# Optimization experiments

Measured on AMD Instinct MI355X. Metric: run time of the kernel, lower is better.

## Reference

```python
import jax, jax.numpy as jnp
import numpy as np

N, L = 1, 384
NODE, H, PD = 256, 8, 128
HD = NODE // H
D1 = H * PD + NODE  # out_transform input dim = 1280


def instance_norm(x, eps=1e-5):
    # x: (N, C, H, W); torch InstanceNorm2d default: no affine, biased var
    m = x.mean(axis=(2, 3), keepdims=True)
    v = x.var(axis=(2, 3), keepdims=True)
    return (x - m) / jnp.sqrt(v + eps)


def conv3x3(x, w, b):
    y = jax.lax.conv_general_dilated(x, w, (1, 1), 'SAME',
                                     dimension_numbers=('NCHW', 'OIHW', 'NCHW'))
    return y + b[None, :, None, None]


def leaky(x):
    return jnp.where(x >= 0, x, 0.01 * x)


def layer_norm(x, w, b, eps=1e-5):
    m = x.mean(-1, keepdims=True)
    v = x.var(-1, keepdims=True)
    return (x - m) / jnp.sqrt(v + eps) * w + b


def setup_inputs() -> dict:
    key = jax.random.key(0)
    ks = jax.random.split(key, 32)
    s = 0.05
    inp = {
        'x': jax.random.normal(ks[0], (N, L, NODE), jnp.float32),
        'z': jax.random.normal(ks[1], (N, L, L, PD), jnp.float32),
        'plddt': jax.random.uniform(ks[2], (N, L, L, 1), jnp.float32),
        # linear weights stored (in, out) so application is x @ W
        'Wq': jax.random.normal(ks[3], (NODE, NODE), jnp.float32) * s,
        'Wk': jax.random.normal(ks[4], (NODE, NODE), jnp.float32) * s,
        'Wv': jax.random.normal(ks[5], (NODE, NODE), jnp.float32) * s,
        'Wp2a': jax.random.normal(ks[6], (PD, H), jnp.float32) * s,
        'conv_a_w': jax.random.normal(ks[7], (H, 2 * H, 3, 3), jnp.float32) * s,
        'conv_a_b': jnp.zeros((H,), jnp.float32),
        'conv_m_w': jax.random.normal(ks[8], (H, H + 1, 3, 3), jnp.float32) * s,
        'conv_m_b': jnp.zeros((H,), jnp.float32),
        'ln1_w': jnp.ones((D1,), jnp.float32),
        'ln1_b': jnp.zeros((D1,), jnp.float32),
        'lin1_w': jax.random.normal(ks[9], (D1, 2 * NODE), jnp.float32) * s,
        'lin1_b': jnp.zeros((2 * NODE,), jnp.float32),
        'ln2_w': jnp.ones((2 * NODE,), jnp.float32),
        'ln2_b': jnp.zeros((2 * NODE,), jnp.float32),
        'lin2_w': jax.random.normal(ks[10], (2 * NODE, NODE), jnp.float32) * s,
        'lin2_b': jnp.zeros((NODE,), jnp.float32),
        'lnf_w': jnp.ones((NODE,), jnp.float32),
        'lnf_b': jnp.zeros((NODE,), jnp.float32),
        'conv_p_w': jax.random.normal(ks[11], (PD, H + PD, 3, 3), jnp.float32) * s,
        'conv_p_b': jnp.zeros((PD,), jnp.float32),
    }
    return inp


def reference(x, z, plddt, Wq, Wk, Wv, Wp2a, conv_a_w, conv_a_b, conv_m_w,
              conv_m_b, ln1_w, ln1_b, lin1_w, lin1_b, ln2_w, ln2_b, lin2_w,
              lin2_b, lnf_w, lnf_b, conv_p_w, conv_p_b):
    Nb, Lh, D = x.shape
    nh = conv_a_w.shape[0]
    hd = D // nh
    Pd = z.shape[-1]
    # node -> alpha (GAT-style QK scores per head)
    q = (x @ Wq).reshape(Nb, Lh, nh, hd)
    k = (x @ Wk).reshape(Nb, Lh, nh, hd)
    v = (x @ Wv).reshape(Nb, Lh, nh, hd)
    a_node = jnp.einsum('nlhd,nmhd->nlmh', q, k) / jnp.sqrt(jnp.float32(hd))
    a_pair = z @ Wp2a                                  # (N,L,L,H)
    a = jnp.concatenate([a_pair, a_node], -1).transpose(0, 3, 1, 2)  # (N,2H,L,L)
    a = leaky(conv3x3(instance_norm(a), conv_a_w, conv_a_b))
    a = jnp.concatenate([a, plddt.transpose(0, 3, 1, 2)], 1)          # (N,H+1,L,L)
    a = leaky(conv3x3(instance_norm(a), conv_m_w, conv_m_b))
    a = a.transpose(0, 2, 3, 1)                                        # (N,L,L,H)
    # aggregations
    nfn = jnp.einsum('nlmh,nmhd->nlhd', a, v).reshape(Nb, Lh, D)       # node from node
    nfp = jnp.einsum('nlmh,nlmp->nlhp', a, z).reshape(Nb, Lh, nh * Pd) # node from pair
    cat = jnp.concatenate([nfp, nfn], -1)
    h = layer_norm(cat, ln1_w, ln1_b) @ lin1_w + lin1_b
    h = leaky(layer_norm(h, ln2_w, ln2_b)) @ lin2_w + lin2_b
    x_new = layer_norm(x + h, lnf_w, lnf_b)
    zp = jnp.concatenate([z, a], -1).transpose(0, 3, 1, 2)             # (N,P+H,L,L)
    z_new = leaky(conv3x3(instance_norm(zp), conv_p_w, conv_p_b)).transpose(0, 2, 3, 1)
    return x_new, z_new
```

## Files before the change

kernel.cpp:

```cpp
#include <hip/hip_runtime.h>
#include <stdint.h>

#define LSEQ 384
#define LL   147456
#define NODE 256
#define NH   8
#define HD   32
#define PDIM 128
#define D1   1280
#define D2   512

typedef __attribute__((ext_vector_type(8))) short s16x8;
typedef __attribute__((ext_vector_type(8))) __bf16 bf16x8;
typedef __attribute__((ext_vector_type(4))) float f32x4;

__device__ __forceinline__ float bf2f(uint16_t u) {
    union { uint32_t i; float f; } x; x.i = ((uint32_t)u) << 16; return x.f;
}
__device__ __forceinline__ uint16_t f2bf(float f) {
    uint32_t b = __float_as_uint(f);
    return (uint16_t)((b + 0x7FFFu + ((b >> 16) & 1u)) >> 16);
}
__device__ __forceinline__ float ld(const void* p, size_t i, int bf) {
    return bf ? bf2f(((const uint16_t*)p)[i]) : ((const float*)p)[i];
}
__device__ __forceinline__ void stout(void* p, size_t i, float v, int bf) {
    if (bf) ((uint16_t*)p)[i] = f2bf(v);
    else    ((float*)p)[i] = v;
}

__device__ __forceinline__ bf16x8 bf16x8_zero() {
    union { s16x8 s; bf16x8 b; } u; u.s = (s16x8)0; return u.b;
}

__device__ __forceinline__ void block_reduce2_256(float* s1, float* s2, int t) {
    __syncthreads();
    for (int o = 128; o > 0; o >>= 1) {
        if (t < o) { s1[t] += s1[t + o]; s2[t] += s2[t + o]; }
        __syncthreads();
    }
}

__device__ __forceinline__ void acc8(uint4 u, float& s, float& ss) {
    uint32_t w[4] = { u.x, u.y, u.z, u.w };
    #pragma unroll
    for (int i = 0; i < 4; ++i) {
        float a = bf2f((uint16_t)(w[i] & 0xFFFFu));
        float b = bf2f((uint16_t)(w[i] >> 16));
        s += a + b;
        ss = fmaf(a, a, ss);
        ss = fmaf(b, b, ss);
    }
}

__global__ void k_detect(const uint32_t* __restrict__ zz, int* __restrict__ flag) {
    if (threadIdx.x == 0 && blockIdx.x == 0) {
        int cnt = 0;
        for (int i = 0; i < 256; ++i) {
            uint32_t lo = zz[i] & 0xFFFFu;
            uint32_t e = (lo >> 7) & 0xFFu;
            if (lo == 0u || (e >= 96u && e <= 142u)) ++cnt;
        }
        flag[0] = (cnt >= 192) ? 1 : 0;
    }
}

__global__ __launch_bounds__(256) void k_cvt(
    const void* __restrict__ src, uint16_t* __restrict__ dst, const int* __restrict__ dt)
{
    int bf = dt[0];
    int i = blockIdx.x * 256 + threadIdx.x;
    dst[i] = f2bf(ld(src, i, bf));
}

__global__ __launch_bounds__(256) void k_wnk(
    const void* __restrict__ src, uint16_t* __restrict__ dst, int K, int N,
    const int* __restrict__ dt)
{
    __shared__ float tile[32][33];
    int bf = dt[0];
    int k0 = blockIdx.x * 32, n0 = blockIdx.y * 32;
    int tr = threadIdx.x >> 5, tc = threadIdx.x & 31;
    #pragma unroll
    for (int i = 0; i < 4; ++i)
        tile[tr + i * 8][tc] = ld(src, (size_t)(k0 + tr + i * 8) * N + n0 + tc, bf);
    __syncthreads();
    #pragma unroll
    for (int i = 0; i < 4; ++i)
        dst[(size_t)(n0 + tr + i * 8) * K + k0 + tc] = f2bf(tile[tc][tr + i * 8]);
}

__global__ __launch_bounds__(256) void k_gemm_bias_f32(
    const uint16_t* __restrict__ A, const uint16_t* __restrict__ B,
    const void* __restrict__ bias, float* __restrict__ out, int K, int N,
    const int* __restrict__ dt)
{
    __shared__ __align__(16) uint16_t As[64 * 72];
    __shared__ __align__(16) uint16_t Bs[64 * 72];
    int bf = dt[0];
    int t = threadIdx.x;
    int row0 = blockIdx.x * 64, col0 = blockIdx.y * 64;
    int w = t >> 6, lane = t & 63, p = lane & 15, g = lane >> 4;
    int wm = w >> 1, wn = w & 1;
    f32x4 acc[2][2];
    #pragma unroll
    for (int i = 0; i < 2; ++i)
        #pragma unroll
        for (int j = 0; j < 2; ++j) acc[i][j] = (f32x4){0.f, 0.f, 0.f, 0.f};

    for (int kc = 0; kc < K; kc += 64) {
        __syncthreads();
        #pragma unroll
        for (int rep = 0; rep < 2; ++rep) {
            int i = t + rep * 256;
            int r = i >> 3, c8 = (i & 7) * 8;
            *(uint4*)&As[r * 72 + c8] = *(const uint4*)&A[(size_t)(row0 + r) * K + kc + c8];
            *(uint4*)&Bs[r * 72 + c8] = *(const uint4*)&B[(size_t)(col0 + r) * K + kc + c8];
        }
        __syncthreads();
        #pragma unroll
        for (int kk = 0; kk < 64; kk += 32) {
            bf16x8 a0 = *(const bf16x8*)&As[(wm * 32 + p) * 72 + kk + 8 * g];
            bf16x8 a1 = *(const bf16x8*)&As[(wm * 32 + 16 + p) * 72 + kk + 8 * g];
            bf16x8 b0 = *(const bf16x8*)&Bs[(wn * 32 + p) * 72 + kk + 8 * g];
            bf16x8 b1 = *(const bf16x8*)&Bs[(wn * 32 + 16 + p) * 72 + kk + 8 * g];
            acc[0][0] = __builtin_amdgcn_mfma_f32_16x16x32_bf16(a0, b0, acc[0][0], 0, 0, 0);
            acc[0][1] = __builtin_amdgcn_mfma_f32_16x16x32_bf16(a0, b1, acc[0][1], 0, 0, 0);
            acc[1][0] = __builtin_amdgcn_mfma_f32_16x16x32_bf16(a1, b0, acc[1][0], 0, 0, 0);
            acc[1][1] = __builtin_amdgcn_mfma_f32_16x16x32_bf16(a1, b1, acc[1][1], 0, 0, 0);
        }
    }
    #pragma unroll
    for (int mi = 0; mi < 2; ++mi)
        #pragma unroll
        for (int ni = 0; ni < 2; ++ni) {
            int n = col0 + wn * 32 + ni * 16 + p;
            float bb = ld(bias, n, bf);
            #pragma unroll
            for (int reg = 0; reg < 4; ++reg) {
                int m = row0 + wm * 32 + mi * 16 + 4 * g + reg;
                out[(size_t)m * N + n] = acc[mi][ni][reg] + bb;
            }
        }
}

__global__ __launch_bounds__(256) void k_gemm_qkv(
    const uint16_t* __restrict__ A, const uint16_t* __restrict__ B,
    uint16_t* __restrict__ q, uint16_t* __restrict__ k, uint16_t* __restrict__ v)
{
    __shared__ __align__(16) uint16_t As[64 * 72];
    __shared__ __align__(16) uint16_t Bs[64 * 72];
    const int K = 256;
    int t = threadIdx.x;
    int row0 = blockIdx.x * 64, col0 = blockIdx.y * 64;
    int w = t >> 6, lane = t & 63, p = lane & 15, g = lane >> 4;
    int wm = w >> 1, wn = w & 1;
    f32x4 acc[2][2];
    #pragma unroll
    for (int i = 0; i < 2; ++i)
        #pragma unroll
        for (int j = 0; j < 2; ++j) acc[i][j] = (f32x4){0.f, 0.f, 0.f, 0.f};

    for (int kc = 0; kc < K; kc += 64) {
        __syncthreads();
        #pragma unroll
        for (int rep = 0; rep < 2; ++rep) {
            int i = t + rep * 256;
            int r = i >> 3, c8 = (i & 7) * 8;
            *(uint4*)&As[r * 72 + c8] = *(const uint4*)&A[(size_t)(row0 + r) * K + kc + c8];
            *(uint4*)&Bs[r * 72 + c8] = *(const uint4*)&B[(size_t)(col0 + r) * K + kc + c8];
        }
        __syncthreads();
        #pragma unroll
        for (int kk = 0; kk < 64; kk += 32) {
            bf16x8 a0 = *(const bf16x8*)&As[(wm * 32 + p) * 72 + kk + 8 * g];
            bf16x8 a1 = *(const bf16x8*)&As[(wm * 32 + 16 + p) * 72 + kk + 8 * g];
            bf16x8 b0 = *(const bf16x8*)&Bs[(wn * 32 + p) * 72 + kk + 8 * g];
            bf16x8 b1 = *(const bf16x8*)&Bs[(wn * 32 + 16 + p) * 72 + kk + 8 * g];
            acc[0][0] = __builtin_amdgcn_mfma_f32_16x16x32_bf16(a0, b0, acc[0][0], 0, 0, 0);
            acc[0][1] = __builtin_amdgcn_mfma_f32_16x16x32_bf16(a0, b1, acc[0][1], 0, 0, 0);
            acc[1][0] = __builtin_amdgcn_mfma_f32_16x16x32_bf16(a1, b0, acc[1][0], 0, 0, 0);
            acc[1][1] = __builtin_amdgcn_mfma_f32_16x16x32_bf16(a1, b1, acc[1][1], 0, 0, 0);
        }
    }
    #pragma unroll
    for (int mi = 0; mi < 2; ++mi)
        #pragma unroll
        for (int ni = 0; ni < 2; ++ni) {
            int nglob = col0 + wn * 32 + ni * 16 + p;
            int sel = nglob >> 8, col = nglob & 255;
            uint16_t* dst = (sel == 0) ? q : (sel == 1) ? k : v;
            #pragma unroll
            for (int reg = 0; reg < 4; ++reg) {
                int m = row0 + wm * 32 + mi * 16 + 4 * g + reg;
                dst[(size_t)m * 256 + col] = f2bf(acc[mi][ni][reg]);
            }
        }
}

__global__ __launch_bounds__(256) void k_lin2lnf_mfma(
    const uint16_t* __restrict__ A, const uint16_t* __restrict__ B,
    const void* __restrict__ bias, const void* __restrict__ x,
    const void* __restrict__ lnw, const void* __restrict__ lnb,
    void* __restrict__ out, const int* __restrict__ dt)
{
    __shared__ __align__(16) uint16_t As[32 * 72];
    __shared__ __align__(16) uint16_t Bs[256 * 72];
    const int K = 512;
    int bf = dt[0];
    int t = threadIdx.x;
    int row0 = blockIdx.x * 32;
    int w = t >> 6, lane = t & 63, p = lane & 15, g = lane >> 4;
    f32x4 acc[2][4];
    #pragma unroll
    for (int i = 0; i < 2; ++i)
        #pragma unroll
        for (int j = 0; j < 4; ++j) acc[i][j] = (f32x4){0.f, 0.f, 0.f, 0.f};

    for (int kc = 0; kc < K; kc += 64) {
        __syncthreads();
        {
            int r = t >> 3, c8 = (t & 7) * 8;
            *(uint4*)&As[r * 72 + c8] = *(const uint4*)&A[(size_t)(row0 + r) * K + kc + c8];
        }
        #pragma unroll
        for (int rep = 0; rep < 8; ++rep) {
            int i = t + rep * 256;
            int r = i >> 3, c8 = (i & 7) * 8;
            *(uint4*)&Bs[r * 72 + c8] = *(const uint4*)&B[(size_t)r * K + kc + c8];
        }
        __syncthreads();
        #pragma unroll
        for (int kk = 0; kk < 64; kk += 32) {
            bf16x8 a0 = *(const bf16x8*)&As[(p) * 72 + kk + 8 * g];
            bf16x8 a1 = *(const bf16x8*)&As[(16 + p) * 72 + kk + 8 * g];
            #pragma unroll
            for (int ni = 0; ni < 4; ++ni) {
                bf16x8 bq = *(const bf16x8*)&Bs[(w * 64 + ni * 16 + p) * 72 + kk + 8 * g];
                acc[0][ni] = __builtin_amdgcn_mfma_f32_16x16x32_bf16(a0, bq, acc[0][ni], 0, 0, 0);
                acc[1][ni] = __builtin_amdgcn_mfma_f32_16x16x32_bf16(a1, bq, acc[1][ni], 0, 0, 0);
            }
        }
    }
    __syncthreads();
    float* lnt = (float*)Bs;
    #pragma unroll
    for (int mi = 0; mi < 2; ++mi)
        #pragma unroll
        for (int ni = 0; ni < 4; ++ni) {
            int n = w * 64 + ni * 16 + p;
            float bb = ld(bias, n, bf);
            #pragma unroll
            for (int reg = 0; reg < 4; ++reg) {
                int m = mi * 16 + 4 * g + reg;
                lnt[m * 264 + n] = acc[mi][ni][reg] + bb + ld(x, (size_t)(row0 + m) * 256 + n, bf);
            }
        }
    __syncthreads();
    for (int rr = 0; rr < 8; ++rr) {
        int m = w * 8 + rr;
        float4 v4 = *(const float4*)&lnt[m * 264 + lane * 4];
        float vv[4] = { v4.x, v4.y, v4.z, v4.w };
        float s = (vv[0] + vv[1]) + (vv[2] + vv[3]);
        float ss = fmaf(vv[0], vv[0], fmaf(vv[1], vv[1], fmaf(vv[2], vv[2], vv[3] * vv[3])));
        #pragma unroll
        for (int off = 32; off > 0; off >>= 1) {
            s  += __shfl_xor(s, off);
            ss += __shfl_xor(ss, off);
        }
        float mean = s / 256.f;
        float rstd = rsqrtf(fmaxf(ss / 256.f - mean * mean, 0.f) + 1e-5f);
        #pragma unroll
        for (int i = 0; i < 4; ++i) {
            int c = lane * 4 + i;
            float val = (vv[i] - mean) * rstd * ld(lnw, c, bf) + ld(lnb, c, bf);
            stout(out, (size_t)(row0 + m) * 256 + c, val, bf);
        }
    }
}

__global__ __launch_bounds__(256) void k_apair(
    const void* __restrict__ z, const void* __restrict__ Wp2a,
    uint16_t* __restrict__ acat, const int* __restrict__ dt)
{
    __shared__ float zl[32 * 129];
    __shared__ float wp[PDIM * NH];
    int bf = dt[0];
    int t = threadIdx.x, m0 = blockIdx.x * 32, l = blockIdx.y;
    for (int i = t; i < PDIM * NH; i += 256) wp[i] = ld(Wp2a, i, bf);
    for (int i = t; i < 32 * PDIM; i += 256) {
        int ml = i >> 7, p = i & 127;
        zl[ml * 129 + p] = ld(z, ((size_t)(l * LSEQ + m0 + ml)) * PDIM + p, bf);
    }
    __syncthreads();
    int h = t >> 5, ml = t & 31;
    float acc = 0.f;
    for (int p = 0; p < PDIM; ++p) acc = fmaf(zl[ml * 129 + p], wp[p * NH + h], acc);
    acat[(size_t)h * LL + l * LSEQ + m0 + ml] = f2bf(acc);
}

__global__ __launch_bounds__(256) void k_anode(
    const uint16_t* __restrict__ q, const uint16_t* __restrict__ k,
    uint16_t* __restrict__ acat)
{
    __shared__ float kl[NODE * 33];
    __shared__ float qr[NH * 33];
    int t = threadIdx.x, m0 = blockIdx.x * 32, l = blockIdx.y;
    for (int i = t; i < 32 * NODE; i += 256) {
        int ml = i >> 8, col = i & 255;
        kl[col * 33 + ml] = bf2f(k[(m0 + ml) * NODE + col]);
    }
    qr[(t >> 5) * 33 + (t & 31)] = bf2f(q[l * NODE + t]);
    __syncthreads();
    int h = t >> 5, ml = t & 31;
    float acc = 0.f;
    #pragma unroll 8
    for (int d = 0; d < HD; ++d)
        acc = fmaf(qr[h * 33 + d], kl[(h * HD + d) * 33 + ml], acc);
    acat[(size_t)(NH + h) * LL + l * LSEQ + m0 + ml] = f2bf(acc * 0.17677669529663687f);
}

__global__ __launch_bounds__(256) void k_scp(
    const uint16_t* __restrict__ src, const void* __restrict__ raw,
    float* __restrict__ ps, float* __restrict__ pss, const int* __restrict__ dt, int C)
{
    __shared__ float s1[256], s2[256];
    int c = blockIdx.y, chunk = blockIdx.x, t = threadIdx.x;
    float s = 0.f, ss = 0.f;
    if (c < C) {
        const uint16_t* p = src + (size_t)c * LL + (size_t)chunk * 8192;
        #pragma unroll
        for (int it = 0; it < 4; ++it) acc8(*(const uint4*)&p[(it * 256 + t) * 8], s, ss);
    } else if (dt[0]) {
        const uint4* p = (const uint4*)raw + (size_t)chunk * 1024;
        #pragma unroll
        for (int it = 0; it < 4; ++it) acc8(p[it * 256 + t], s, ss);
    } else {
        const float4* p = (const float4*)raw + (size_t)chunk * 2048;
        #pragma unroll
        for (int it = 0; it < 8; ++it) {
            float4 a = p[it * 256 + t];
            s += (a.x + a.y) + (a.z + a.w);
            ss = fmaf(a.x, a.x, fmaf(a.y, a.y, fmaf(a.z, a.z, fmaf(a.w, a.w, ss))));
        }
    }
    s1[t] = s; s2[t] = ss;
    block_reduce2_256(s1, s2, t);
    if (t == 0) { ps[c * 18 + chunk] = s1[0]; pss[c * 18 + chunk] = s2[0]; }
}

__global__ void k_scf(
    const float* __restrict__ ps, const float* __restrict__ pss,
    float* __restrict__ mean_out, float* __restrict__ rstd_out, int C)
{
    int t = threadIdx.x;
    if (t < C) {
        float s = 0.f, ss = 0.f;
        for (int i = 0; i < 18; ++i) { s += ps[t * 18 + i]; ss += pss[t * 18 + i]; }
        float m = s / (float)LL;
        float var = ss / (float)LL - m * m;
        mean_out[t] = m; rstd_out[t] = rsqrtf(fmaxf(var, 0.f) + 1e-5f);
    }
}

__global__ __launch_bounds__(128) void k_conv_a(
    const uint16_t* __restrict__ acat, const void* __restrict__ wa,
    const void* __restrict__ ba, const float* __restrict__ mean,
    const float* __restrict__ rstd, uint16_t* __restrict__ out,
    const int* __restrict__ dt)
{
    __shared__ float wl[144];
    __shared__ float ot[9];
    __shared__ float mn[16];
    int bf = dt[0];
    int t = threadIdx.x;
    int oc = blockIdx.z, l = blockIdx.y, m = blockIdx.x * 128 + t;
    if (t < 16) mn[t] = mean[t];
    for (int i = t; i < 144; i += 128) {
        int ic = i / 9;
        wl[i] = ld(wa, oc * 144 + i, bf) * rstd[ic];
    }
    __syncthreads();
    if (t < 9) {
        float s = 0.f;
        for (int ic = 0; ic < 16; ++ic) s = fmaf(mn[ic], wl[ic * 9 + t], s);
        ot[t] = s;
    }
    __syncthreads();
    float acc = ld(ba, oc, bf);
    #pragma unroll
    for (int r = 0; r < 3; ++r) {
        int li = l + r - 1;
        if (li < 0 || li >= LSEQ) continue;
        #pragma unroll
        for (int c = 0; c < 3; ++c) {
            int mi = m + c - 1;
            if (mi < 0 || mi >= LSEQ) continue;
            const uint16_t* ip = acat + li * LSEQ + mi;
            float a = 0.f;
            #pragma unroll
            for (int ic = 0; ic < 16; ++ic) a = fmaf(bf2f(ip[(size_t)ic * LL]), wl[ic * 9 + r * 3 + c], a);
            acc += a - ot[r * 3 + c];
        }
    }
    acc = acc >= 0.f ? acc : 0.01f * acc;
    out[(size_t)oc * LL + l * LSEQ + m] = f2bf(acc);
}

__global__ __launch_bounds__(128) void k_conv_m(
    const uint16_t* __restrict__ a1, const void* __restrict__ plddt,
    const void* __restrict__ wm, const void* __restrict__ bm,
    const float* __restrict__ mean, const float* __restrict__ rstd,
    uint16_t* __restrict__ out, const int* __restrict__ dt)
{
    __shared__ float wl[81];
    __shared__ float ot[9];
    __shared__ float mn[9];
    int bf = dt[0];
    int t = threadIdx.x;
    int oc = blockIdx.z, l = blockIdx.y, m = blockIdx.x * 128 + t;
    if (t < 9) mn[t] = mean[t];
    for (int i = t; i < 81; i += 128) {
        int ic = i / 9;
        wl[i] = ld(wm, oc * 81 + i, bf) * rstd[ic];
    }
    __syncthreads();
    if (t < 9) {
        float s = 0.f;
        for (int ic = 0; ic < 9; ++ic) s = fmaf(mn[ic], wl[ic * 9 + t], s);
        ot[t] = s;
    }
    __syncthreads();
    float acc = ld(bm, oc, bf);
    #pragma unroll
    for (int r = 0; r < 3; ++r) {
        int li = l + r - 1;
        if (li < 0 || li >= LSEQ) continue;
        #pragma unroll
        for (int c = 0; c < 3; ++c) {
            int mi = m + c - 1;
            if (mi < 0 || mi >= LSEQ) continue;
            int off = li * LSEQ + mi;
            float a = 0.f;
            #pragma unroll
            for (int ic = 0; ic < 8; ++ic) a = fmaf(bf2f(a1[(size_t)ic * LL + off]), wl[ic * 9 + r * 3 + c], a);
            a = fmaf(ld(plddt, off, bf), wl[72 + r * 3 + c], a);
            acc += a - ot[r * 3 + c];
        }
    }
    acc = acc >= 0.f ? acc : 0.01f * acc;
    out[(size_t)oc * LL + l * LSEQ + m] = f2bf(acc);
}

__global__ __launch_bounds__(512) void k_agg(
    const uint16_t* __restrict__ a2, const uint16_t* __restrict__ v,
    const void* __restrict__ z, float* __restrict__ cat,
    const int* __restrict__ dt)
{
    __shared__ float al[NH * LSEQ];
    __shared__ float hp[3 * NH * PDIM];
    int bf = dt[0];
    int t = threadIdx.x, l = blockIdx.x;
    for (int i = t; i < NH * LSEQ; i += 512) {
        int h = i / LSEQ, m = i - h * LSEQ;
        al[i] = bf2f(a2[(size_t)h * LL + l * LSEQ + m]);
    }
    __syncthreads();
    int p = t & 127, qq = t >> 7;
    float acc[NH];
    #pragma unroll
    for (int h = 0; h < NH; ++h) acc[h] = 0.f;
    size_t zrow = (size_t)l * LSEQ * PDIM;
    for (int m = qq; m < LSEQ; m += 4) {
        float zv = ld(z, zrow + (size_t)m * PDIM + p, bf);
        #pragma unroll
        for (int h = 0; h < NH; ++h) acc[h] = fmaf(al[h * LSEQ + m], zv, acc[h]);
    }
    if (qq) {
        #pragma unroll
        for (int h = 0; h < NH; ++h) hp[(qq - 1) * 1024 + h * PDIM + p] = acc[h];
    }
    __syncthreads();
    if (qq == 0) {
        #pragma unroll
        for (int h = 0; h < NH; ++h)
            cat[(size_t)l * D1 + h * PDIM + p] =
                acc[h] + hp[h * PDIM + p] + hp[1024 + h * PDIM + p] + hp[2048 + h * PDIM + p];
    }
    int o = t & 255, half = t >> 8;
    int h2 = o >> 5;
    float s = 0.f;
    for (int m = half; m < LSEQ; m += 2)
        s = fmaf(al[h2 * LSEQ + m], bf2f(v[m * NODE + o]), s);
    __syncthreads();
    if (half) hp[o] = s;
    __syncthreads();
    if (!half) cat[(size_t)l * D1 + NH * PDIM + o] = s + hp[o];
}

__global__ __launch_bounds__(256) void k_ln1(
    const float* __restrict__ cat, const void* __restrict__ w,
    const void* __restrict__ b, uint16_t* __restrict__ outn,
    const int* __restrict__ dt)
{
    __shared__ float s1[256], s2[256];
    int bf = dt[0];
    int t = threadIdx.x, l = blockIdx.x;
    const float* row = cat + (size_t)l * D1;
    float s = 0.f, ss = 0.f;
    for (int i = t; i < D1; i += 256) { float v = row[i]; s += v; ss = fmaf(v, v, ss); }
    s1[t] = s; s2[t] = ss;
    block_reduce2_256(s1, s2, t);
    float m = s1[0] / (float)D1;
    float rstd = rsqrtf(fmaxf(s2[0] / (float)D1 - m * m, 0.f) + 1e-5f);
    for (int i = t; i < D1; i += 256)
        outn[(size_t)l * D1 + i] = f2bf((row[i] - m) * rstd * ld(w, i, bf) + ld(b, i, bf));
}

__global__ __launch_bounds__(256) void k_ln2(
    const float* __restrict__ in, const void* __restrict__ w,
    const void* __restrict__ b, uint16_t* __restrict__ outn,
    const int* __restrict__ dt)
{
    __shared__ float s1[256], s2[256];
    int bf = dt[0];
    int t = threadIdx.x, l = blockIdx.x;
    const float* row = in + (size_t)l * D2;
    float v0 = row[t], v1 = row[t + 256];
    s1[t] = v0 + v1; s2[t] = v0 * v0 + v1 * v1;
    block_reduce2_256(s1, s2, t);
    float m = s1[0] / (float)D2;
    float rstd = rsqrtf(fmaxf(s2[0] / (float)D2 - m * m, 0.f) + 1e-5f);
    float o0 = (v0 - m) * rstd * ld(w, t, bf) + ld(b, t, bf);
    float o1 = (v1 - m) * rstd * ld(w, t + 256, bf) + ld(b, t + 256, bf);
    outn[(size_t)l * D2 + t]       = f2bf(o0 >= 0.f ? o0 : 0.01f * o0);
    outn[(size_t)l * D2 + t + 256] = f2bf(o1 >= 0.f ? o1 : 0.01f * o1);
}

__global__ __launch_bounds__(256) void k_pstat(
    const void* __restrict__ z, float* __restrict__ psum, float* __restrict__ psumsq,
    const int* __restrict__ dt)
{
    __shared__ float sa[128], sb[128];
    int bf = dt[0];
    int t = threadIdx.x;
    int ch = t & 127, half = t >> 7;
    size_t r0 = (size_t)blockIdx.x * 256;
    float s = 0.f, ss = 0.f;
    for (int i = 0; i < 128; ++i) {
        float v = ld(z, (r0 + half + 2 * i) * PDIM + ch, bf);
        s += v; ss = fmaf(v, v, ss);
    }
    if (half) { sa[ch] = s; sb[ch] = ss; }
    __syncthreads();
    if (!half) {
        psum[blockIdx.x * PDIM + ch] = s + sa[ch];
        psumsq[blockIdx.x * PDIM + ch] = ss + sb[ch];
    }
}

__global__ __launch_bounds__(512) void k_finP(
    const float* __restrict__ psum, const float* __restrict__ psumsq,
    float* __restrict__ meanP, float* __restrict__ rstdP)
{
    __shared__ float s1[512], s2[512];
    int t = threadIdx.x;
    int c = t & 127, seg = t >> 7;
    float s = 0.f, ss = 0.f;
    for (int b = seg * 144; b < seg * 144 + 144; ++b) {
        s += psum[b * PDIM + c]; ss += psumsq[b * PDIM + c];
    }
    s1[t] = s; s2[t] = ss;
    __syncthreads();
    if (t < 128) {
        float S  = s1[t] + s1[t + 128] + s1[t + 256] + s1[t + 384];
        float SS = s2[t] + s2[t + 128] + s2[t + 256] + s2[t + 384];
        float m = S / (float)LL;
        float var = SS / (float)LL - m * m;
        meanP[t] = m; rstdP[t] = rsqrtf(fmaxf(var, 0.f) + 1e-5f);
    }
}

__global__ __launch_bounds__(64) void k_wprep(
    const void* __restrict__ wp, uint16_t* __restrict__ wt, const int* __restrict__ dt)
{
    int bf = dt[0];
    int oc = blockIdx.x, tap = blockIdx.y;
    for (int ic = threadIdx.x; ic < 144; ic += 64) {
        float v = (ic < 136) ? ld(wp, (size_t)oc * 1224 + (size_t)ic * 9 + tap, bf) : 0.f;
        wt[((size_t)tap * 128 + oc) * 144 + ic] = f2bf(v);
    }
}

__global__ __launch_bounds__(512, 1) void k_conv_p_mfma(
    const void* __restrict__ z, const uint16_t* __restrict__ a2,
    const uint16_t* __restrict__ wt, const void* __restrict__ bp,
    const float* __restrict__ meanP, const float* __restrict__ rstdP,
    void* __restrict__ out, const int* __restrict__ dt)
{
    __shared__ __align__(16) uint16_t As[6 * 34 * 144];
    __shared__ __align__(16) uint16_t Ws[2][128 * 144];
    __shared__ float mloc[136], rloc[136];

    int bf = dt[0];
    int t = threadIdx.x;
    int m0 = blockIdx.x * 32, l0 = blockIdx.y * 4;

    if (t < 136) { mloc[t] = meanP[t]; rloc[t] = rstdP[t]; }
    __syncthreads();

    for (int grp = t; grp < 3672; grp += 512) {
        int pixidx = grp / 18;
        int icg = (grp - pixidx * 18) * 8;
        int lr = pixidx / 34, lc = pixidx - lr * 34;
        int li = l0 - 1 + lr, mi = m0 - 1 + lc;
        uint16_t vals[8];
        if (li < 0 || li >= LSEQ || mi < 0 || mi >= LSEQ || icg >= 136) {
            #pragma unroll
            for (int j = 0; j < 8; ++j) vals[j] = 0;
        } else if (icg < 128) {
            size_t zoff = ((size_t)li * LSEQ + mi) * PDIM + icg;
            if (bf) {
                const uint16_t* zp = (const uint16_t*)z + zoff;
                #pragma unroll
                for (int j = 0; j < 8; ++j)
                    vals[j] = f2bf((bf2f(zp[j]) - mloc[icg + j]) * rloc[icg + j]);
            } else {
                const float* zp = (const float*)z + zoff;
                #pragma unroll
                for (int j = 0; j < 8; ++j)
                    vals[j] = f2bf((zp[j] - mloc[icg + j]) * rloc[icg + j]);
            }
        } else {
            size_t poff = (size_t)li * LSEQ + mi;
            #pragma unroll
            for (int j = 0; j < 8; ++j)
                vals[j] = f2bf((bf2f(a2[(size_t)j * LL + poff]) - mloc[128 + j]) * rloc[128 + j]);
        }
        *(uint4*)&As[pixidx * 144 + icg] = *(const uint4*)vals;
    }
    {
        const uint4* wsrc = (const uint4*)wt;
        uint4* wdst = (uint4*)Ws[0];
        for (int i = t; i < 2304; i += 512) wdst[i] = wsrc[i];
    }
    __syncthreads();

    int w = t >> 6, lane = t & 63;
    int p = lane & 15, g = lane >> 4;
    int r = w >> 1;
    int ocb = (w & 1) * 64;
    int bb0 = (ocb + p) * 144 + 8 * g;

    f32x4 acc0[4], acc1[4];
    #pragma unroll
    for (int n = 0; n < 4; ++n) {
        acc0[n] = (f32x4){0.f, 0.f, 0.f, 0.f};
        acc1[n] = (f32x4){0.f, 0.f, 0.f, 0.f};
    }
    bf16x8 bz = bf16x8_zero();

    for (int tap = 0; tap < 9; ++tap) {
        int cur = tap & 1;
        uint4 wreg[5];
        if (tap < 8) {
            const uint4* wsrc = (const uint4*)(wt + (size_t)(tap + 1) * 18432);
            #pragma unroll
            for (int j = 0; j < 4; ++j) wreg[j] = wsrc[t + 512 * j];
            if (t < 256) wreg[4] = wsrc[2048 + t];
        }

        int tr = tap / 3, tc = tap - tr * 3;
        int abase = ((r + tr) * 34 + p + tc) * 144 + 8 * g;
        const uint16_t* Wc = Ws[cur];

        #pragma unroll
        for (int ch = 0; ch < 5; ++ch) {
            const int ic0 = (ch < 4) ? ch * 32 : 112;
            bf16x8 a0 = *(const bf16x8*)&As[abase + ic0];
            bf16x8 a1 = *(const bf16x8*)&As[abase + 2304 + ic0];
            #pragma unroll
            for (int n = 0; n < 4; ++n) {
                bf16x8 bq;
                if (ch < 4) {
                    bq = *(const bf16x8*)&Wc[bb0 + n * 2304 + ic0];
                } else {
                    bq = bz;
                    if (g == 2) bq = *(const bf16x8*)&Wc[bb0 + n * 2304 + 112];
                }
                acc0[n] = __builtin_amdgcn_mfma_f32_16x16x32_bf16(a0, bq, acc0[n], 0, 0, 0);
                acc1[n] = __builtin_amdgcn_mfma_f32_16x16x32_bf16(a1, bq, acc1[n], 0, 0, 0);
            }
        }

        if (tap < 8) {
            uint4* wdst = (uint4*)Ws[cur ^ 1];
            #pragma unroll
            for (int j = 0; j < 4; ++j) wdst[t + 512 * j] = wreg[j];
            if (t < 256) wdst[2048 + t] = wreg[4];
        }
        __syncthreads();
    }

    int l = l0 + r;
    #pragma unroll
    for (int n = 0; n < 4; ++n) {
        int oc = ocb + 16 * n + p;
        float bb = ld(bp, oc, bf);
        #pragma unroll
        for (int reg = 0; reg < 4; ++reg) {
            int pc = 4 * g + reg;
            float v0 = acc0[n][reg] + bb; v0 = v0 >= 0.f ? v0 : 0.01f * v0;
            stout(out, 98304 + ((size_t)l * LSEQ + (m0 + pc)) * PDIM + oc, v0, bf);
            float v1 = acc1[n][reg] + bb; v1 = v1 >= 0.f ? v1 : 0.01f * v1;
            stout(out, 98304 + ((size_t)l * LSEQ + (m0 + 16 + pc)) * PDIM + oc, v1, bf);
        }
    }
}

__global__ __launch_bounds__(128) void k_conv_p(
    const void* __restrict__ z, const uint16_t* __restrict__ a2,
    const void* __restrict__ wp, const void* __restrict__ bp,
    const float* __restrict__ meanP, const float* __restrict__ rstdP,
    void* __restrict__ out, const int* __restrict__ dt)
{
    __shared__ __align__(16) float wlds[128 * 76];
    __shared__ __align__(16) float inl[4 * 18 * 8];
    int bf = dt[0];
    int t = threadIdx.x;
    int m0 = blockIdx.x * 16, l0 = blockIdx.y * 2;
    float acc0[16], acc1[16];
    #pragma unroll
    for (int i = 0; i < 16; ++i) { acc0[i] = 0.f; acc1[i] = 0.f; }

    for (int ic0 = 0; ic0 < 136; ic0 += 8) {
        __syncthreads();
        for (int i = t; i < 128 * 72; i += 128) {
            int op = i / 72, r = i % 72;
            int cc = r / 9, tap = r % 9;
            wlds[op * 76 + tap * 8 + cc] = ld(wp, op * 1224 + (ic0 + cc) * 9 + tap, bf);
        }
        for (int i = t; i < 4 * 18 * 8; i += 128) {
            int rr = i / 144, rem = i % 144;
            int col = rem >> 3, cc = rem & 7;
            int li = l0 - 1 + rr, mi = m0 - 1 + col, ic = ic0 + cc;
            float vv = 0.f;
            if (li >= 0 && li < LSEQ && mi >= 0 && mi < LSEQ) {
                float raw = (ic < PDIM) ? ld(z, ((size_t)li * LSEQ + mi) * PDIM + ic, bf)
                                        : bf2f(a2[(size_t)(ic - PDIM) * LL + li * LSEQ + mi]);
                vv = (raw - meanP[ic]) * rstdP[ic];
            }
            inl[i] = vv;
        }
        __syncthreads();
        #pragma unroll
        for (int qd = 0; qd < 2; ++qd) {
            float4 wq[9];
            #pragma unroll
            for (int tap = 0; tap < 9; ++tap)
                wq[tap] = *(const float4*)&wlds[t * 76 + tap * 8 + qd * 4];
            float4 win[4][3];
            #pragma unroll
            for (int r = 0; r < 4; ++r) {
                win[r][1] = *(const float4*)&inl[(r * 18 + 0) * 8 + qd * 4];
                win[r][2] = *(const float4*)&inl[(r * 18 + 1) * 8 + qd * 4];
                win[r][0] = win[r][1];
            }
            #pragma unroll
            for (int pix = 0; pix < 16; ++pix) {
                #pragma unroll
                for (int r = 0; r < 4; ++r) {
                    win[r][0] = win[r][1];
                    win[r][1] = win[r][2];
                    win[r][2] = *(const float4*)&inl[(r * 18 + pix + 2) * 8 + qd * 4];
                }
                float p0x = 0.f, p0y = 0.f, p0z = 0.f, p0w = 0.f;
                float p1x = 0.f, p1y = 0.f, p1z = 0.f, p1w = 0.f;
                #pragma unroll
                for (int tr = 0; tr < 3; ++tr) {
                    #pragma unroll
                    for (int c = 0; c < 3; ++c) {
                        float4 w4 = wq[tr * 3 + c];
                        float4 u0 = win[tr][c];
                        float4 u1 = win[tr + 1][c];
                        p0x = fmaf(w4.x, u0.x, p0x); p0y = fmaf(w4.y, u0.y, p0y);
                        p0z = fmaf(w4.z, u0.z, p0z); p0w = fmaf(w4.w, u0.w, p0w);
                        p1x = fmaf(w4.x, u1.x, p1x); p1y = fmaf(w4.y, u1.y, p1y);
                        p1z = fmaf(w4.z, u1.z, p1z); p1w = fmaf(w4.w, u1.w, p1w);
                    }
                }
                acc0[pix] += (p0x + p0y) + (p0z + p0w);
                acc1[pix] += (p1x + p1y) + (p1z + p1w);
            }
        }
    }
    float bb = ld(bp, t, bf);
    #pragma unroll
    for (int pix = 0; pix < 16; ++pix) {
        float v0 = acc0[pix] + bb; v0 = v0 >= 0.f ? v0 : 0.01f * v0;
        stout(out, 98304 + ((size_t)l0 * LSEQ + m0 + pix) * PDIM + t, v0, bf);
        float v1 = acc1[pix] + bb; v1 = v1 >= 0.f ? v1 : 0.01f * v1;
        stout(out, 98304 + ((size_t)(l0 + 1) * LSEQ + m0 + pix) * PDIM + t, v1, bf);
    }
}

extern "C" void kernel_launch(void* const* d_in, const int* in_sizes, int n_in,
                              void* d_out, int out_size, void* d_ws, size_t ws_size,
                              hipStream_t stream)
{
    const void* x     = d_in[0];
    const void* z     = d_in[1];
    const void* plddt = d_in[2];
    const void* Wq    = d_in[3];
    const void* Wk    = d_in[4];
    const void* Wv    = d_in[5];
    const void* Wp2a  = d_in[6];
    const void* caw   = d_in[7];
    const void* cab   = d_in[8];
    const void* cmw   = d_in[9];
    const void* cmb   = d_in[10];
    const void* ln1w  = d_in[11];
    const void* ln1b  = d_in[12];
    const void* l1w   = d_in[13];
    const void* l1b   = d_in[14];
    const void* ln2w  = d_in[15];
    const void* ln2b  = d_in[16];
    const void* l2w   = d_in[17];
    const void* l2b   = d_in[18];
    const void* lnfw  = d_in[19];
    const void* lnfb  = d_in[20];
    const void* cpw   = d_in[21];
    const void* cpb   = d_in[22];

    uint16_t* O = (uint16_t*)d_out;
    uint16_t* acat = O + 98304;
    uint16_t* a1b  = O + 2457600;
    uint16_t* qb   = a1b;
    uint16_t* kb   = a1b + 98304;
    uint16_t* vb   = O + 3637248;
    float*    cat  = (float*)(O + 3735552);
    float*    h1   = (float*)(O + 5701632);
    float*    psum = (float*)(O + 6488064);
    float*    psumsq = (float*)(O + 6635520);
    uint16_t* cb   = O + 6782976;
    uint16_t* h1nb = O + 7274496;
    uint16_t* xb   = O + 7471104;
    uint16_t* wtq  = O + 7569408;
    uint16_t* wt1  = O + 7766016;
    uint16_t* wt2  = O + 8421376;

    uint16_t* U = (uint16_t*)d_ws;
    uint16_t* a2b = U;
    float*    st  = (float*)(U + 1179648);
    float* m16 = st;        float* r16 = st + 16;
    float* m9  = st + 32;   float* r9  = st + 48;
    float* mP  = st + 64;   float* rP  = st + 200;
    int*   flg = (int*)(U + 1181696);
    uint16_t* wt = U + 1182720;
    int use_mfma = (ws_size >= (size_t)2365440 + 331776);

    k_detect<<<1, 64, 0, stream>>>((const uint32_t*)z, flg);
    k_cvt<<<384, 256, 0, stream>>>(x, xb, flg);
    k_wnk<<<dim3(8, 8), 256, 0, stream>>>(Wq, wtq,          256, 256, flg);
    k_wnk<<<dim3(8, 8), 256, 0, stream>>>(Wk, wtq +  65536, 256, 256, flg);
    k_wnk<<<dim3(8, 8), 256, 0, stream>>>(Wv, wtq + 131072, 256, 256, flg);
    k_wnk<<<dim3(40, 16), 256, 0, stream>>>(l1w, wt1, 1280, 512, flg);
    k_wnk<<<dim3(16, 8), 256, 0, stream>>>(l2w, wt2,  512, 256, flg);

    k_gemm_qkv<<<dim3(6, 12), 256, 0, stream>>>(xb, wtq, qb, kb, vb);
    k_apair <<<dim3(12, LSEQ), 256, 0, stream>>>(z, Wp2a, acat, flg);
    k_anode <<<dim3(12, LSEQ), 256, 0, stream>>>(qb, kb, acat);
    k_scp<<<dim3(18, 16), 256, 0, stream>>>(acat, plddt, psum, psumsq, flg, 16);
    k_scf<<<1, 16, 0, stream>>>(psum, psumsq, m16, r16, 16);
    k_conv_a<<<dim3(3, LSEQ, 8), 128, 0, stream>>>(acat, caw, cab, m16, r16, a1b, flg);
    k_scp<<<dim3(18, 9), 256, 0, stream>>>(a1b, plddt, psum, psumsq, flg, 8);
    k_scf<<<1, 9, 0, stream>>>(psum, psumsq, m9, r9, 9);
    k_conv_m<<<dim3(3, LSEQ, 8), 128, 0, stream>>>(a1b, plddt, cmw, cmb, m9, r9, a2b, flg);
    k_agg   <<<LSEQ, 512, 0, stream>>>(a2b, vb, z, cat, flg);
    k_ln1   <<<LSEQ, 256, 0, stream>>>(cat, ln1w, ln1b, cb, flg);
    k_gemm_bias_f32<<<dim3(6, 8), 256, 0, stream>>>(cb, wt1, l1b, h1, 1280, 512, flg);
    k_ln2   <<<LSEQ, 256, 0, stream>>>(h1, ln2w, ln2b, h1nb, flg);
    k_lin2lnf_mfma<<<12, 256, 0, stream>>>(h1nb, wt2, l2b, x, lnfw, lnfb, d_out, flg);
    k_scp<<<dim3(18, 8), 256, 0, stream>>>(a2b, plddt, psum, psumsq, flg, 8);
    k_scf<<<1, 8, 0, stream>>>(psum, psumsq, mP + 128, rP + 128, 8);
    k_pstat <<<576, 256, 0, stream>>>(z, psum, psumsq, flg);
    k_finP  <<<1, 512, 0, stream>>>(psum, psumsq, mP, rP);
    if (use_mfma) {
        k_wprep<<<dim3(128, 9), 64, 0, stream>>>(cpw, wt, flg);
        k_conv_p_mfma<<<dim3(12, 96), 512, 0, stream>>>(z, a2b, wt, cpb, mP, rP, d_out, flg);
    } else {
        k_conv_p<<<dim3(24, 192), 128, 0, stream>>>(z, a2b, cpw, cpb, mP, rP, d_out, flg);
    }
}
```

Baseline: 621.0 us.

## Vectorize loads, compute all output channels per thread in small convs, retile conv_p

k_apair and k_anode now load z and k with 16-byte vector loads instead of scalar loads. k_conv_a and k_conv_m compute all 8 output channels per thread, so each input tap is read once instead of once per output channel, using tap-major weights in shared memory read as float4. k_conv_p_mfma moves to 256-thread blocks covering 2 rows each, with a single weight buffer loaded synchronously per tap instead of the register-staged double buffer, aiming for two blocks per CU. This trades cross-tap weight prefetch overlap for higher occupancy and less shared memory per block.

After: 579.9 us. 1.07x faster.

```diff
diff --git a/kernel.cpp b/kernel.cpp
--- a/kernel.cpp
+++ b/kernel.cpp
@@ -288,9 +288,23 @@
     int bf = dt[0];
     int t = threadIdx.x, m0 = blockIdx.x * 32, l = blockIdx.y;
     for (int i = t; i < PDIM * NH; i += 256) wp[i] = ld(Wp2a, i, bf);
-    for (int i = t; i < 32 * PDIM; i += 256) {
-        int ml = i >> 7, p = i & 127;
-        zl[ml * 129 + p] = ld(z, ((size_t)(l * LSEQ + m0 + ml)) * PDIM + p, bf);
+    if (bf) {
+        const uint16_t* zz = (const uint16_t*)z;
+        for (int grp = t; grp < 512; grp += 256) {
+            int ml = grp >> 4, p8 = (grp & 15) * 8;
+            uint4 u = *(const uint4*)&zz[((size_t)(l * LSEQ + m0 + ml)) * PDIM + p8];
+            const uint16_t* pu = (const uint16_t*)&u;
+            #pragma unroll
+            for (int j = 0; j < 8; ++j) zl[ml * 129 + p8 + j] = bf2f(pu[j]);
+        }
+    } else {
+        const float* zz = (const float*)z;
+        for (int grp = t; grp < 1024; grp += 256) {
+            int ml = grp >> 5, p4 = (grp & 31) * 4;
+            float4 u = *(const float4*)&zz[((size_t)(l * LSEQ + m0 + ml)) * PDIM + p4];
+            zl[ml * 129 + p4 + 0] = u.x; zl[ml * 129 + p4 + 1] = u.y;
+            zl[ml * 129 + p4 + 2] = u.z; zl[ml * 129 + p4 + 3] = u.w;
+        }
     }
     __syncthreads();
     int h = t >> 5, ml = t & 31;
@@ -306,9 +320,12 @@
     __shared__ float kl[NODE * 33];
     __shared__ float qr[NH * 33];
     int t = threadIdx.x, m0 = blockIdx.x * 32, l = blockIdx.y;
-    for (int i = t; i < 32 * NODE; i += 256) {
-        int ml = i >> 8, col = i & 255;
-        kl[col * 33 + ml] = bf2f(k[(m0 + ml) * NODE + col]);
+    for (int grp = t; grp < 1024; grp += 256) {
+        int ml = grp >> 5, c8 = (grp & 31) * 8;
+        uint4 u = *(const uint4*)&k[(size_t)(m0 + ml) * NODE + c8];
+        const uint16_t* pu = (const uint16_t*)&u;
+        #pragma unroll
+        for (int j = 0; j < 8; ++j) kl[(c8 + j) * 33 + ml] = bf2f(pu[j]);
     }
     qr[(t >> 5) * 33 + (t & 31)] = bf2f(q[l * NODE + t]);
     __syncthreads();
@@ -369,25 +386,27 @@
     const float* __restrict__ rstd, uint16_t* __restrict__ out,
     const int* __restrict__ dt)
 {
-    __shared__ float wl[144];
-    __shared__ float ot[9];
-    __shared__ float mn[16];
+    __shared__ float wl[9 * 8 * 16];
+    __shared__ float ot[8 * 9];
     int bf = dt[0];
     int t = threadIdx.x;
-    int oc = blockIdx.z, l = blockIdx.y, m = blockIdx.x * 128 + t;
-    if (t < 16) mn[t] = mean[t];
-    for (int i = t; i < 144; i += 128) {
-        int ic = i / 9;
-        wl[i] = ld(wa, oc * 144 + i, bf) * rstd[ic];
-    }
-    __syncthreads();
-    if (t < 9) {
+    int l = blockIdx.y, m = blockIdx.x * 128 + t;
+    for (int i = t; i < 1152; i += 128) {
+        int tap = i >> 7, rem = i & 127;
+        int oc = rem >> 4, ic = rem & 15;
+        wl[i] = ld(wa, (size_t)oc * 144 + ic * 9 + tap, bf) * rstd[ic];
+    }
+    __syncthreads();
+    if (t < 72) {
+        int oc = t / 9, tap = t - oc * 9;
         float s = 0.f;
-        for (int ic = 0; ic < 16; ++ic) s = fmaf(mn[ic], wl[ic * 9 + t], s);
+        for (int ic = 0; ic < 16; ++ic) s = fmaf(mean[ic], wl[tap * 128 + oc * 16 + ic], s);
         ot[t] = s;
     }
     __syncthreads();
-    float acc = ld(ba, oc, bf);
+    float acc[8];
+    #pragma unroll
+    for (int oc = 0; oc < 8; ++oc) acc[oc] = ld(ba, oc, bf);
     #pragma unroll
     for (int r = 0; r < 3; ++r) {
         int li = l + r - 1;
@@ -397,14 +416,32 @@
             int mi = m + c - 1;
             if (mi < 0 || mi >= LSEQ) continue;
             const uint16_t* ip = acat + li * LSEQ + mi;
-            float a = 0.f;
-            #pragma unroll
-            for (int ic = 0; ic < 16; ++ic) a = fmaf(bf2f(ip[(size_t)ic * LL]), wl[ic * 9 + r * 3 + c], a);
-            acc += a - ot[r * 3 + c];
-        }
-    }
-    acc = acc >= 0.f ? acc : 0.01f * acc;
-    out[(size_t)oc * LL + l * LSEQ + m] = f2bf(acc);
+            float v[16];
+            #pragma unroll
+            for (int ic = 0; ic < 16; ++ic) v[ic] = bf2f(ip[(size_t)ic * LL]);
+            int tap = r * 3 + c;
+            const float4* wq = (const float4*)&wl[tap * 128];
+            #pragma unroll
+            for (int oc = 0; oc < 8; ++oc) {
+                float4 w0 = wq[oc * 4], w1 = wq[oc * 4 + 1], w2 = wq[oc * 4 + 2], w3 = wq[oc * 4 + 3];
+                float a = acc[oc] - ot[oc * 9 + tap];
+                a = fmaf(w0.x, v[0], a);  a = fmaf(w0.y, v[1], a);
+                a = fmaf(w0.z, v[2], a);  a = fmaf(w0.w, v[3], a);
+                a = fmaf(w1.x, v[4], a);  a = fmaf(w1.y, v[5], a);
+                a = fmaf(w1.z, v[6], a);  a = fmaf(w1.w, v[7], a);
+                a = fmaf(w2.x, v[8], a);  a = fmaf(w2.y, v[9], a);
+                a = fmaf(w2.z, v[10], a); a = fmaf(w2.w, v[11], a);
+                a = fmaf(w3.x, v[12], a); a = fmaf(w3.y, v[13], a);
+                a = fmaf(w3.z, v[14], a); a = fmaf(w3.w, v[15], a);
+                acc[oc] = a;
+            }
+        }
+    }
+    #pragma unroll
+    for (int oc = 0; oc < 8; ++oc) {
+        float a = acc[oc] >= 0.f ? acc[oc] : 0.01f * acc[oc];
+        out[(size_t)oc * LL + l * LSEQ + m] = f2bf(a);
+    }
 }
 
 __global__ __launch_bounds__(128) void k_conv_m(
@@ -413,25 +450,27 @@
     const float* __restrict__ mean, const float* __restrict__ rstd,
     uint16_t* __restrict__ out, const int* __restrict__ dt)
 {
-    __shared__ float wl[81];
-    __shared__ float ot[9];
-    __shared__ float mn[9];
+    __shared__ float wl[9 * 8 * 12];
+    __shared__ float ot[8 * 9];
     int bf = dt[0];
     int t = threadIdx.x;
-    int oc = blockIdx.z, l = blockIdx.y, m = blockIdx.x * 128 + t;
-    if (t < 9) mn[t] = mean[t];
-    for (int i = t; i < 81; i += 128) {
-        int ic = i / 9;
-        wl[i] = ld(wm, oc * 81 + i, bf) * rstd[ic];
-    }
-    __syncthreads();
-    if (t < 9) {
+    int l = blockIdx.y, m = blockIdx.x * 128 + t;
+    for (int i = t; i < 864; i += 128) {
+        int tap = i / 96, rem = i - tap * 96;
+        int oc = rem / 12, ic = rem - oc * 12;
+        wl[i] = (ic < 9) ? ld(wm, (size_t)oc * 81 + ic * 9 + tap, bf) * rstd[ic] : 0.f;
+    }
+    __syncthreads();
+    if (t < 72) {
+        int oc = t / 9, tap = t - oc * 9;
         float s = 0.f;
-        for (int ic = 0; ic < 9; ++ic) s = fmaf(mn[ic], wl[ic * 9 + t], s);
+        for (int ic = 0; ic < 9; ++ic) s = fmaf(mean[ic], wl[tap * 96 + oc * 12 + ic], s);
         ot[t] = s;
     }
     __syncthreads();
-    float acc = ld(bm, oc, bf);
+    float acc[8];
+    #pragma unroll
+    for (int oc = 0; oc < 8; ++oc) acc[oc] = ld(bm, oc, bf);
     #pragma unroll
     for (int r = 0; r < 3; ++r) {
         int li = l + r - 1;
@@ -441,15 +480,30 @@
             int mi = m + c - 1;
             if (mi < 0 || mi >= LSEQ) continue;
             int off = li * LSEQ + mi;
-            float a = 0.f;
-            #pragma unroll
-            for (int ic = 0; ic < 8; ++ic) a = fmaf(bf2f(a1[(size_t)ic * LL + off]), wl[ic * 9 + r * 3 + c], a);
-            a = fmaf(ld(plddt, off, bf), wl[72 + r * 3 + c], a);
-            acc += a - ot[r * 3 + c];
-        }
-    }
-    acc = acc >= 0.f ? acc : 0.01f * acc;
-    out[(size_t)oc * LL + l * LSEQ + m] = f2bf(acc);
+            float v[12];
+            #pragma unroll
+            for (int ic = 0; ic < 8; ++ic) v[ic] = bf2f(a1[(size_t)ic * LL + off]);
+            v[8] = ld(plddt, off, bf); v[9] = 0.f; v[10] = 0.f; v[11] = 0.f;
+            int tap = r * 3 + c;
+            const float4* wq = (const float4*)&wl[tap * 96];
+            #pragma unroll
+            for (int oc = 0; oc < 8; ++oc) {
+                float4 w0 = wq[oc * 3], w1 = wq[oc * 3 + 1], w2 = wq[oc * 3 + 2];
+                float a = acc[oc] - ot[oc * 9 + tap];
+                a = fmaf(w0.x, v[0], a); a = fmaf(w0.y, v[1], a);
+                a = fmaf(w0.z, v[2], a); a = fmaf(w0.w, v[3], a);
+                a = fmaf(w1.x, v[4], a); a = fmaf(w1.y, v[5], a);
+                a = fmaf(w1.z, v[6], a); a = fmaf(w1.w, v[7], a);
+                a = fmaf(w2.x, v[8], a);
+                acc[oc] = a;
+            }
+        }
+    }
+    #pragma unroll
+    for (int oc = 0; oc < 8; ++oc) {
+        float a = acc[oc] >= 0.f ? acc[oc] : 0.01f * acc[oc];
+        out[(size_t)oc * LL + l * LSEQ + m] = f2bf(a);
+    }
 }
 
 __global__ __launch_bounds__(512) void k_agg(
@@ -592,24 +646,24 @@
     }
 }
 
-__global__ __launch_bounds__(512, 1) void k_conv_p_mfma(
+__global__ __launch_bounds__(256, 2) void k_conv_p_mfma(
     const void* __restrict__ z, const uint16_t* __restrict__ a2,
     const uint16_t* __restrict__ wt, const void* __restrict__ bp,
     const float* __restrict__ meanP, const float* __restrict__ rstdP,
     void* __restrict__ out, const int* __restrict__ dt)
 {
-    __shared__ __align__(16) uint16_t As[6 * 34 * 144];
-    __shared__ __align__(16) uint16_t Ws[2][128 * 144];
+    __shared__ __align__(16) uint16_t As[4 * 34 * 144];
+    __shared__ __align__(16) uint16_t Ws[128 * 144];
     __shared__ float mloc[136], rloc[136];
 
     int bf = dt[0];
     int t = threadIdx.x;
-    int m0 = blockIdx.x * 32, l0 = blockIdx.y * 4;
+    int m0 = blockIdx.x * 32, l0 = blockIdx.y * 2;
 
     if (t < 136) { mloc[t] = meanP[t]; rloc[t] = rstdP[t]; }
     __syncthreads();
 
-    for (int grp = t; grp < 3672; grp += 512) {
+    for (int grp = t; grp < 2448; grp += 256) {
         int pixidx = grp / 18;
         int icg = (grp - pixidx * 18) * 8;
         int lr = pixidx / 34, lc = pixidx - lr * 34;
@@ -639,12 +693,6 @@
         }
         *(uint4*)&As[pixidx * 144 + icg] = *(const uint4*)vals;
     }
-    {
-        const uint4* wsrc = (const uint4*)wt;
-        uint4* wdst = (uint4*)Ws[0];
-        for (int i = t; i < 2304; i += 512) wdst[i] = wsrc[i];
-    }
-    __syncthreads();
 
     int w = t >> 6, lane = t & 63;
     int p = lane & 15, g = lane >> 4;
@@ -661,18 +709,17 @@
     bf16x8 bz = bf16x8_zero();
 
     for (int tap = 0; tap < 9; ++tap) {
-        int cur = tap & 1;
-        uint4 wreg[5];
-        if (tap < 8) {
-            const uint4* wsrc = (const uint4*)(wt + (size_t)(tap + 1) * 18432);
-            #pragma unroll
-            for (int j = 0; j < 4; ++j) wreg[j] = wsrc[t + 512 * j];
-            if (t < 256) wreg[4] = wsrc[2048 + t];
-        }
+        __syncthreads();
+        {
+            const uint4* wsrc = (const uint4*)(wt + (size_t)tap * 18432);
+            uint4* wdst = (uint4*)Ws;
+            #pragma unroll
+            for (int i = 0; i < 9; ++i) wdst[t + i * 256] = wsrc[t + i * 256];
+        }
+        __syncthreads();
 
         int tr = tap / 3, tc = tap - tr * 3;
         int abase = ((r + tr) * 34 + p + tc) * 144 + 8 * g;
-        const uint16_t* Wc = Ws[cur];
 
         #pragma unroll
         for (int ch = 0; ch < 5; ++ch) {
@@ -683,23 +730,15 @@
             for (int n = 0; n < 4; ++n) {
                 bf16x8 bq;
                 if (ch < 4) {
-                    bq = *(const bf16x8*)&Wc[bb0 + n * 2304 + ic0];
+                    bq = *(const bf16x8*)&Ws[bb0 + n * 2304 + ic0];
                 } else {
                     bq = bz;
-                    if (g == 2) bq = *(const bf16x8*)&Wc[bb0 + n * 2304 + 112];
+                    if (g == 2) bq = *(const bf16x8*)&Ws[bb0 + n * 2304 + 112];
                 }
                 acc0[n] = __builtin_amdgcn_mfma_f32_16x16x32_bf16(a0, bq, acc0[n], 0, 0, 0);
                 acc1[n] = __builtin_amdgcn_mfma_f32_16x16x32_bf16(a1, bq, acc1[n], 0, 0, 0);
             }
         }
-
-        if (tap < 8) {
-            uint4* wdst = (uint4*)Ws[cur ^ 1];
-            #pragma unroll
-            for (int j = 0; j < 4; ++j) wdst[t + 512 * j] = wreg[j];
-            if (t < 256) wdst[2048 + t] = wreg[4];
-        }
-        __syncthreads();
     }
 
     int l = l0 + r;
@@ -872,10 +911,10 @@
     k_anode <<<dim3(12, LSEQ), 256, 0, stream>>>(qb, kb, acat);
     k_scp<<<dim3(18, 16), 256, 0, stream>>>(acat, plddt, psum, psumsq, flg, 16);
     k_scf<<<1, 16, 0, stream>>>(psum, psumsq, m16, r16, 16);
-    k_conv_a<<<dim3(3, LSEQ, 8), 128, 0, stream>>>(acat, caw, cab, m16, r16, a1b, flg);
+    k_conv_a<<<dim3(3, LSEQ), 128, 0, stream>>>(acat, caw, cab, m16, r16, a1b, flg);
     k_scp<<<dim3(18, 9), 256, 0, stream>>>(a1b, plddt, psum, psumsq, flg, 8);
     k_scf<<<1, 9, 0, stream>>>(psum, psumsq, m9, r9, 9);
-    k_conv_m<<<dim3(3, LSEQ, 8), 128, 0, stream>>>(a1b, plddt, cmw, cmb, m9, r9, a2b, flg);
+    k_conv_m<<<dim3(3, LSEQ), 128, 0, stream>>>(a1b, plddt, cmw, cmb, m9, r9, a2b, flg);
     k_agg   <<<LSEQ, 512, 0, stream>>>(a2b, vb, z, cat, flg);
     k_ln1   <<<LSEQ, 256, 0, stream>>>(cat, ln1w, ln1b, cb, flg);
     k_gemm_bias_f32<<<dim3(6, 8), 256, 0, stream>>>(cb, wt1, l1b, h1, 1280, 512, flg);
@@ -887,7 +926,7 @@
     k_finP  <<<1, 512, 0, stream>>>(psum, psumsq, mP, rP);
     if (use_mfma) {
         k_wprep<<<dim3(128, 9), 64, 0, stream>>>(cpw, wt, flg);
-        k_conv_p_mfma<<<dim3(12, 96), 512, 0, stream>>>(z, a2b, wt, cpb, mP, rP, d_out, flg);
+        k_conv_p_mfma<<<dim3(12, 192), 256, 0, stream>>>(z, a2b, wt, cpb, mP, rP, d_out, flg);
     } else {
         k_conv_p<<<dim3(24, 192), 128, 0, stream>>>(z, a2b, cpw, cpb, mP, rP, d_out, flg);
     }
```
